# Performance work log

Measured on AMD Instinct MI355X. Metric: run time of the kernel, lower is better.

## Reference

```python
import jax, jax.numpy as jnp
import numpy as np

N = 100000       # nodes
F_IN = 512       # input features
H = 16           # hidden dim of conv1
C = 5            # num classes
E = 6400000      # edges (avg degree 64)


def setup_inputs() -> dict:
    key = jax.random.key(0)
    ks = jax.random.split(key, 8)
    x = jax.random.normal(ks[0], (N, F_IN), dtype=jnp.float32)
    edge_index = jax.random.randint(ks[1], (2, E), 0, N, dtype=jnp.int64)
    W1 = jax.random.normal(ks[2], (F_IN, H), dtype=jnp.float32) * (1.0 / np.sqrt(F_IN))
    b1 = jnp.zeros((H,), jnp.float32)
    W2 = jax.random.normal(ks[3], (H, C), dtype=jnp.float32) * (1.0 / np.sqrt(H))
    b2 = jnp.zeros((C,), jnp.float32)
    W3 = jax.random.normal(ks[4], (C, 32), dtype=jnp.float32) * (1.0 / np.sqrt(C))
    b3 = jnp.zeros((32,), jnp.float32)
    W4 = jax.random.normal(ks[5], (32, C), dtype=jnp.float32) * (1.0 / np.sqrt(32))
    b4 = jnp.zeros((C,), jnp.float32)
    return {"x": x, "edge_index": edge_index, "W1": W1, "b1": b1,
            "W2": W2, "b2": b2, "W3": W3, "b3": b3, "W4": W4, "b4": b4}


def _gcn_norm(edge_index):
    # add self-loops, unit edge weights (data has no edge_attr)
    loop = jnp.arange(N, dtype=edge_index.dtype)
    src = jnp.concatenate([edge_index[0], loop])
    dst = jnp.concatenate([edge_index[1], loop])
    deg = jax.ops.segment_sum(jnp.ones_like(dst, dtype=jnp.float32), dst,
                              num_segments=N)
    dinv = jnp.where(deg > 0, jax.lax.rsqrt(jnp.maximum(deg, 1.0)), 0.0)
    norm = dinv[src] * dinv[dst]  # [E+N]
    return src, dst, norm


def _gcn_conv(x, src, dst, norm, W, b):
    h = x @ W                               # transform first (small out dim)
    msg = h[src] * norm[:, None]            # gather + edge-normalize
    out = jax.ops.segment_sum(msg, dst, num_segments=N)  # scatter-add
    return out + b


def reference(x, edge_index, W1, b1, W2, b2, W3, b3, W4, b4):
    src, dst, norm = _gcn_norm(edge_index)
    h = _gcn_conv(x, src, dst, norm, W1, b1)
    h = jax.nn.relu(h)
    # F.dropout(training=self.training): identity in eval mode
    h = _gcn_conv(h, src, dst, norm, W2, b2)
    h = jax.nn.relu(h @ W3 + b3)
    h = h @ W4 + b4
    return jax.nn.log_softmax(h, axis=1)
```

## Files before the change

kernel.cpp:

```cpp
#include <hip/hip_runtime.h>
#include <hip/hip_bf16.h>


#define F_IN 512
#define HDIM 16
#define CDIM 5
#define NB   1024
#define SEG  8192
#define GWP_STRIDE 16
#define SCHUNK 12288
#define CAP  8192

typedef __attribute__((ext_vector_type(8))) short short8;
typedef __attribute__((ext_vector_type(4))) float floatx4;

__device__ inline float bf2f(unsigned short u){
  unsigned int i = ((unsigned int)u) << 16; float f; __builtin_memcpy(&f, &i, 4); return f;
}
__device__ inline unsigned short f2bf(float x){
  unsigned int i; __builtin_memcpy(&i, &x, 4);
  unsigned int r = i + 0x7FFFu + ((i >> 16) & 1u);
  return (unsigned short)(r >> 16);
}
__device__ inline float ulo(unsigned int u){
  unsigned int v = u << 16; float f; __builtin_memcpy(&f, &v, 4); return f;
}
__device__ inline float uhi(unsigned int u){
  unsigned int v = u & 0xFFFF0000u; float f; __builtin_memcpy(&f, &v, 4); return f;
}
__device__ inline short8 pack8(float4 u0, float4 u1){
  unsigned short o[8] = {f2bf(u0.x), f2bf(u0.y), f2bf(u0.z), f2bf(u0.w),
                         f2bf(u1.x), f2bf(u1.y), f2bf(u1.z), f2bf(u1.w)};
  short8 r; __builtin_memcpy(&r, o, 16); return r;
}

__global__ void k_detect(const int* __restrict__ ei, int* __restrict__ flag,
                         int* __restrict__ gwp, int E){
  int k = blockIdx.x * blockDim.x + threadIdx.x;
  if (k < NB) gwp[k * GWP_STRIDE] = k * SEG;
  long long step = E / 2048; if (step < 1) step = 1;
  long long pos = 2LL * ((long long)k * step) + 1;
  if (pos < 2LL * E){
    if (ei[pos] != 0) atomicOr(flag, 1);
  }
}

__global__ __launch_bounds__(1024) void k_binscatter(const int* __restrict__ ei, const int* __restrict__ flag,
                                                     int* __restrict__ gwp, int* __restrict__ pairs,
                                                     int E, int NPB){
  __shared__ int bh[NB];
  __shared__ int lex[NB + 1];
  __shared__ int bb2[NB];
  __shared__ int wsum[16];
  __shared__ int stage[SCHUNK];
  int t = threadIdx.x;
  int e0 = blockIdx.x * SCHUNK;
  int e1 = min(E, e0 + SCHUNK);
  int cnt = e1 - e0;
  if (cnt <= 0) return;
  int is32 = *flag;
  const uint2* ei2 = (const uint2*)ei;
  bh[t] = 0;
  __syncthreads();
  for (int e = e0 + t; e < e1; e += 1024){
    int dst = is32 ? ei[(size_t)E + e] : (int)ei2[(size_t)E + e].x;
    atomicAdd(&bh[dst / NPB], 1);
  }
  __syncthreads();
  {
    int lane = t & 63, w = t >> 6;
    int v = bh[t];
    int xs = v;
    #pragma unroll
    for (int off = 1; off < 64; off <<= 1){
      int y = __shfl_up(xs, off);
      if (lane >= off) xs += y;
    }
    if (lane == 63) wsum[w] = xs;
    __syncthreads();
    int woff = 0;
    for (int k = 0; k < w; ++k) woff += wsum[k];
    int excl = woff + xs - v;
    lex[t] = excl;
    if (t == 1023) lex[NB] = woff + xs;
    bb2[t] = v ? atomicAdd(&gwp[t * GWP_STRIDE], v) : 0;
    __syncthreads();
    bh[t] = excl;
  }
  __syncthreads();
  for (int e = e0 + t; e < e1; e += 1024){
    int src, dst;
    if (is32){ src = ei[e]; dst = ei[(size_t)E + e]; }
    else     { src = (int)ei2[e].x; dst = (int)ei2[(size_t)E + e].x; }
    int b = dst / NPB;
    int dl = dst - b * NPB;
    int idx = atomicAdd(&bh[b], 1);
    stage[idx] = src | (dl << 20);
  }
  __syncthreads();
  for (int k = t; k < cnt; k += 1024){
    int lo = 0, hi = NB;
    while (hi - lo > 1){
      int mid = (lo + hi) >> 1;
      if (lex[mid] <= k) lo = mid; else hi = mid;
    }
    pairs[bb2[lo] + (k - lex[lo])] = stage[k];
  }
}

__global__ __launch_bounds__(1024) void k_scanNB(const int* __restrict__ gwp, int* __restrict__ bbase,
                                                 int nb){
  __shared__ int wsum[16];
  int t = threadIdx.x, lane = t & 63, w = t >> 6;
  int v = (t < nb) ? (gwp[t * GWP_STRIDE] - t * SEG) : 0;
  int xs = v;
  #pragma unroll
  for (int off = 1; off < 64; off <<= 1){
    int y = __shfl_up(xs, off);
    if (lane >= off) xs += y;
  }
  if (lane == 63) wsum[w] = xs;
  __syncthreads();
  int woff = 0;
  for (int k = 0; k < w; ++k) woff += wsum[k];
  if (t < nb) bbase[t] = woff + xs - v;
  if (t == 1023) bbase[nb] = woff + xs;
}

__global__ __launch_bounds__(512) void k_bucket(const int* __restrict__ pairs, const int* __restrict__ bbase,
                                                int* __restrict__ rowptr, float* __restrict__ dinv,
                                                int* __restrict__ ssrc, int NPB, int n, int Etot){
  __shared__ int lcnt[4][128];
  __shared__ int tot[128];
  __shared__ int lexcl[129];
  __shared__ int stage[CAP];
  int b = blockIdx.x;
  int t = threadIdx.x;
  int g = t >> 7;
  int node0 = b * NPB;
  int pbase = b * SEG;
  int obase = bbase[b];
  int cntE = bbase[b + 1] - obase;
  lcnt[g][t & 127] = 0;
  __syncthreads();
  for (int k = t; k < cntE; k += 512){
    unsigned int v = (unsigned int)pairs[pbase + k];
    atomicAdd(&lcnt[g][v >> 20], 1);
  }
  __syncthreads();
  if (t < 128){
    int s0 = lcnt[0][t], s1 = lcnt[1][t], s2 = lcnt[2][t], s3 = lcnt[3][t];
    tot[t] = s0 + s1 + s2 + s3;
    lcnt[0][t] = 0; lcnt[1][t] = s0; lcnt[2][t] = s0 + s1; lcnt[3][t] = s0 + s1 + s2;
  }
  __syncthreads();
  if (t == 0){
    int s = 0;
    for (int k = 0; k < NPB; ++k){ lexcl[k] = s; s += tot[k]; }
    lexcl[NPB] = s;
  }
  __syncthreads();
  if (t < NPB){
    int node = node0 + t;
    if (node < n){
      rowptr[node] = obase + lexcl[t];
      dinv[node] = rsqrtf((float)(tot[t] + 1));
    }
  }
  lcnt[g][t & 127] += lexcl[t & 127];
  if (b == 0 && t == 0) rowptr[n] = Etot;
  __syncthreads();
  for (int k = t; k < cntE; k += 512){
    unsigned int v = (unsigned int)pairs[pbase + k];
    int idx = atomicAdd(&lcnt[g][v >> 20], 1);
    int src = (int)(v & 0xFFFFFu);
    if (idx < CAP) stage[idx] = src;
    else ssrc[obase + idx] = src;
  }
  __syncthreads();
  int m = cntE < CAP ? cntE : CAP;
  for (int k = t; k < m; k += 512) ssrc[obase + k] = stage[k];
}

__global__ __launch_bounds__(256) void k_gemm1(const float* __restrict__ x, const float* __restrict__ W1,
                                               const float* __restrict__ dinv, unsigned short* __restrict__ hs1,
                                               int n){
  int lane = threadIdx.x & 63;
  int col = lane & 15;
  int kg  = lane >> 4;
  int nt = (n + 15) >> 4;
  short8 B[16];
  #pragma unroll
  for (int t = 0; t < 16; ++t){
    unsigned short o[8];
    #pragma unroll
    for (int e = 0; e < 8; ++e)
      o[e] = f2bf(W1[(t * 32 + kg * 8 + e) * HDIM + col]);
    __builtin_memcpy(&B[t], o, 16);
  }
  int nw = gridDim.x * 4;
  for (int wid = blockIdx.x * 4 + (threadIdx.x >> 6); wid < nt; wid += nw){
    int row = wid * 16 + col;
    const float* xr = x + (size_t)min(row, n - 1) * F_IN;
    floatx4 acc = {0.f, 0.f, 0.f, 0.f};
    #pragma unroll
    for (int t = 0; t < 16; ++t){
      const float4* p = (const float4*)(xr + t * 32 + kg * 8);
      float4 u0 = p[0];
      float4 u1 = p[1];
      acc = __builtin_amdgcn_mfma_f32_16x16x32_bf16(pack8(u0, u1), B[t], acc, 0, 0, 0);
    }
    #pragma unroll
    for (int r = 0; r < 4; ++r){
      int orow = wid * 16 + kg * 4 + r;
      if (orow < n) hs1[(size_t)orow * HDIM + col] = f2bf(dinv[orow] * acc[r]);
    }
  }
}

__global__ __launch_bounds__(256) void k_agg1(const unsigned short* __restrict__ hs1,
    const int* __restrict__ rowptr, const int* __restrict__ ssrc,
    const float* __restrict__ dinv, const float* __restrict__ b1,
    const float* __restrict__ W2, unsigned short* __restrict__ hs2, int n){
  int lane = threadIdx.x & 63;
  int i = blockIdx.x * 4 + (threadIdx.x >> 6);
  if (i >= n) return;
  int slot = lane >> 1, half = lane & 1;
  int beg = rowptr[i], end = rowptr[i + 1];
  const uint4* hv = (const uint4*)hs1;
  float acc[8];
  #pragma unroll
  for (int k = 0; k < 8; ++k) acc[k] = 0.f;
  for (int e = beg + slot; e < end; e += 32){
    int src = ssrc[e];
    uint4 v = hv[(size_t)src * 2 + half];
    acc[0] += ulo(v.x); acc[1] += uhi(v.x);
    acc[2] += ulo(v.y); acc[3] += uhi(v.y);
    acc[4] += ulo(v.z); acc[5] += uhi(v.z);
    acc[6] += ulo(v.w); acc[7] += uhi(v.w);
  }
  #pragma unroll
  for (int off = 2; off < 64; off <<= 1){
    #pragma unroll
    for (int k = 0; k < 8; ++k) acc[k] += __shfl_xor(acc[k], off);
  }
  uint4 sv = hv[(size_t)i * 2 + half];
  float self[8] = {ulo(sv.x), uhi(sv.x), ulo(sv.y), uhi(sv.y),
                   ulo(sv.z), uhi(sv.z), ulo(sv.w), uhi(sv.w)};
  float dv = dinv[i];
  const float4* b1v = (const float4*)b1;
  float4 bl = b1v[half * 2], bh = b1v[half * 2 + 1];
  float r[8];
  r[0] = fmaxf(fmaf(dv, acc[0] + self[0], bl.x), 0.f);
  r[1] = fmaxf(fmaf(dv, acc[1] + self[1], bl.y), 0.f);
  r[2] = fmaxf(fmaf(dv, acc[2] + self[2], bl.z), 0.f);
  r[3] = fmaxf(fmaf(dv, acc[3] + self[3], bl.w), 0.f);
  r[4] = fmaxf(fmaf(dv, acc[4] + self[4], bh.x), 0.f);
  r[5] = fmaxf(fmaf(dv, acc[5] + self[5], bh.y), 0.f);
  r[6] = fmaxf(fmaf(dv, acc[6] + self[6], bh.z), 0.f);
  r[7] = fmaxf(fmaf(dv, acc[7] + self[7], bh.w), 0.f);
  const float* w2 = W2 + half * 8 * CDIM;
  float p[CDIM];
  #pragma unroll
  for (int c = 0; c < CDIM; ++c){
    float s = 0.f;
    #pragma unroll
    for (int k = 0; k < 8; ++k) s = fmaf(r[k], w2[k * CDIM + c], s);
    p[c] = s;
  }
  #pragma unroll
  for (int c = 0; c < CDIM; ++c) p[c] += __shfl_xor(p[c], 1);
  if (lane == 0){
    unsigned short o[8];
    #pragma unroll
    for (int c = 0; c < CDIM; ++c) o[c] = f2bf(dv * p[c]);
    o[5] = 0; o[6] = 0; o[7] = 0;
    uint4 v; __builtin_memcpy(&v, o, 16);
    *(uint4*)(hs2 + (size_t)i * 8) = v;
  }
}

__global__ __launch_bounds__(256) void k_agg2(const unsigned short* __restrict__ hs2,
    const int* __restrict__ rowptr, const int* __restrict__ ssrc,
    const float* __restrict__ dinv, const float* __restrict__ b2,
    const float* __restrict__ W3, const float* __restrict__ b3,
    const float* __restrict__ W4, const float* __restrict__ b4,
    float* __restrict__ out, int n){
  int lane = threadIdx.x & 63;
  int i = blockIdx.x * 4 + (threadIdx.x >> 6);
  if (i >= n) return;
  int beg = rowptr[i], end = rowptr[i + 1];
  const uint4* hv = (const uint4*)hs2;
  float acc[CDIM];
  #pragma unroll
  for (int k = 0; k < CDIM; ++k) acc[k] = 0.f;
  for (int e = beg + lane; e < end; e += 64){
    int src = ssrc[e];
    uint4 v = hv[src];
    acc[0] += ulo(v.x); acc[1] += uhi(v.x);
    acc[2] += ulo(v.y); acc[3] += uhi(v.y);
    acc[4] += ulo(v.z);
  }
  #pragma unroll
  for (int off = 1; off < 64; off <<= 1){
    #pragma unroll
    for (int k = 0; k < CDIM; ++k) acc[k] += __shfl_xor(acc[k], off);
  }
  float dv = dinv[i];
  uint4 sv = hv[i];
  float a0 = fmaf(dv, acc[0] + ulo(sv.x), b2[0]);
  float a1 = fmaf(dv, acc[1] + uhi(sv.x), b2[1]);
  float a2 = fmaf(dv, acc[2] + ulo(sv.y), b2[2]);
  float a3 = fmaf(dv, acc[3] + uhi(sv.y), b2[3]);
  float a4 = fmaf(dv, acc[4] + ulo(sv.z), b2[4]);
  int m = lane & 31;
  float h3 = b3[m];
  h3 = fmaf(a0, W3[0 * 32 + m], h3);
  h3 = fmaf(a1, W3[1 * 32 + m], h3);
  h3 = fmaf(a2, W3[2 * 32 + m], h3);
  h3 = fmaf(a3, W3[3 * 32 + m], h3);
  h3 = fmaf(a4, W3[4 * 32 + m], h3);
  h3 = fmaxf(h3, 0.f);
  float q0 = h3 * W4[m * CDIM + 0], q1 = h3 * W4[m * CDIM + 1], q2 = h3 * W4[m * CDIM + 2];
  float q3 = h3 * W4[m * CDIM + 3], q4 = h3 * W4[m * CDIM + 4];
  #pragma unroll
  for (int off = 1; off < 32; off <<= 1){
    q0 += __shfl_xor(q0, off); q1 += __shfl_xor(q1, off); q2 += __shfl_xor(q2, off);
    q3 += __shfl_xor(q3, off); q4 += __shfl_xor(q4, off);
  }
  q0 += b4[0]; q1 += b4[1]; q2 += b4[2]; q3 += b4[3]; q4 += b4[4];
  float mx = fmaxf(fmaxf(fmaxf(q0, q1), fmaxf(q2, q3)), q4);
  float sum = expf(q0 - mx) + expf(q1 - mx) + expf(q2 - mx) + expf(q3 - mx) + expf(q4 - mx);
  float lse = mx + logf(sum);
  if (lane < CDIM){
    float v = q0;
    if (lane == 1) v = q1;
    if (lane == 2) v = q2;
    if (lane == 3) v = q3;
    if (lane == 4) v = q4;
    out[(size_t)i * CDIM + lane] = v - lse;
  }
}

extern "C" void kernel_launch(void* const* d_in, const int* in_sizes, int n_in,
                              void* d_out, int out_size, void* d_ws, size_t ws_size,
                              hipStream_t stream){
  const float* x  = (const float*)d_in[0];
  const int*   ei = (const int*)d_in[1];
  const float* W1 = (const float*)d_in[2];
  const float* b1 = (const float*)d_in[3];
  const float* W2 = (const float*)d_in[4];
  const float* b2 = (const float*)d_in[5];
  const float* W3 = (const float*)d_in[6];
  const float* b3 = (const float*)d_in[7];
  const float* W4 = (const float*)d_in[8];
  const float* b4 = (const float*)d_in[9];
  float* out = (float*)d_out;

  int N = in_sizes[0] / F_IN;
  int E = in_sizes[1] / 2;
  int NPB = (N + NB - 1) / NB;

  char* ws = (char*)d_ws;
  size_t off = 0;
  auto alloc = [&](size_t bytes) -> char* {
    char* p = ws + off;
    off += (bytes + 255) & ~(size_t)255;
    return p;
  };
  int* flag  = (int*)alloc(4);
  int* gwp   = (int*)alloc((size_t)NB * GWP_STRIDE * 4);
  int* bbase = (int*)alloc(((size_t)NB + 1) * 4);
  int* rowptr= (int*)alloc(((size_t)N + 1) * 4);
  float* dinv= (float*)alloc((size_t)N * 4);
  int* pairs = (int*)alloc((size_t)NB * SEG * 4);
  int* ssrc  = (int*)alloc((size_t)E * 4);
  unsigned short* hs1 = (unsigned short*)alloc((size_t)N * HDIM * 2);
  unsigned short* hs2 = (unsigned short*)alloc((size_t)N * 8 * 2);
  (void)ws_size; (void)n_in; (void)out_size;

  hipMemsetAsync(flag, 0, 4, stream);
  k_detect<<<8, 256, 0, stream>>>(ei, flag, gwp, E);
  int sblocks = (E + SCHUNK - 1) / SCHUNK;
  k_binscatter<<<sblocks, 1024, 0, stream>>>(ei, flag, gwp, pairs, E, NPB);
  k_scanNB<<<1, 1024, 0, stream>>>(gwp, bbase, NB);
  k_bucket<<<NB, 512, 0, stream>>>(pairs, bbase, rowptr, dinv, ssrc, NPB, N, E);
  k_gemm1<<<768, 256, 0, stream>>>(x, W1, dinv, hs1, N);
  k_agg1<<<(N + 3) / 4, 256, 0, stream>>>(hs1, rowptr, ssrc, dinv, b1, W2, hs2, N);
  k_agg2<<<(N + 3) / 4, 256, 0, stream>>>(hs2, rowptr, ssrc, dinv, b2, W3, b3, W4, b4, out, N);
}
```

Baseline: 282.3 us.

## Load edges once into registers in binscatter, parallel scan in bucket, drop memset

The binscatter kernel now reads each edge's src/dst once into per-thread register arrays (12 per thread) and reuses them for both the histogram and scatter passes, instead of reading edge_index twice from global memory. The bucket kernel replaces a serial single-thread prefix sum over node counts with a wave-shuffle scan. The flag memset is folded into a single-block detect kernel, removing one launch. The register arrays raise register pressure in a 1024-thread block, and the in-kernel flag clear relies on __syncthreads ordering within that one block.

```diff
diff --git a/kernel.cpp b/kernel.cpp
--- a/kernel.cpp
+++ b/kernel.cpp
@@ -8,7 +8,8 @@
 #define NB   1024
 #define SEG  8192
 #define GWP_STRIDE 16
-#define SCHUNK 12288
+#define EPT  12
+#define SCHUNK (1024*EPT)
 #define CAP  8192
 
 typedef __attribute__((ext_vector_type(8))) short short8;
@@ -34,12 +35,14 @@
   short8 r; __builtin_memcpy(&r, o, 16); return r;
 }
 
-__global__ void k_detect(const int* __restrict__ ei, int* __restrict__ flag,
-                         int* __restrict__ gwp, int E){
-  int k = blockIdx.x * blockDim.x + threadIdx.x;
-  if (k < NB) gwp[k * GWP_STRIDE] = k * SEG;
-  long long step = E / 2048; if (step < 1) step = 1;
-  long long pos = 2LL * ((long long)k * step) + 1;
+__global__ __launch_bounds__(1024) void k_detect(const int* __restrict__ ei, int* __restrict__ flag,
+                                                 int* __restrict__ gwp, int E){
+  int t = threadIdx.x;
+  if (t == 0) *flag = 0;
+  gwp[t * GWP_STRIDE] = t * SEG;
+  __syncthreads();
+  long long step = E / 1024; if (step < 1) step = 1;
+  long long pos = 2LL * ((long long)t * step) + 1;
   if (pos < 2LL * E){
     if (ei[pos] != 0) atomicOr(flag, 1);
   }
@@ -60,12 +63,23 @@
   if (cnt <= 0) return;
   int is32 = *flag;
   const uint2* ei2 = (const uint2*)ei;
+  int pk[EPT]; int bi[EPT];
+  #pragma unroll
+  for (int j = 0; j < EPT; ++j){
+    int e = e0 + t + j * 1024;
+    if (e < e1){
+      int src, dst;
+      if (is32){ src = ei[e]; dst = ei[(size_t)E + e]; }
+      else     { src = (int)ei2[e].x; dst = (int)ei2[(size_t)E + e].x; }
+      int b = dst / NPB;
+      pk[j] = src | ((dst - b * NPB) << 20);
+      bi[j] = b;
+    } else bi[j] = -1;
+  }
   bh[t] = 0;
   __syncthreads();
-  for (int e = e0 + t; e < e1; e += 1024){
-    int dst = is32 ? ei[(size_t)E + e] : (int)ei2[(size_t)E + e].x;
-    atomicAdd(&bh[dst / NPB], 1);
-  }
+  #pragma unroll
+  for (int j = 0; j < EPT; ++j) if (bi[j] >= 0) atomicAdd(&bh[bi[j]], 1);
   __syncthreads();
   {
     int lane = t & 63, w = t >> 6;
@@ -88,14 +102,12 @@
     bh[t] = excl;
   }
   __syncthreads();
-  for (int e = e0 + t; e < e1; e += 1024){
-    int src, dst;
-    if (is32){ src = ei[e]; dst = ei[(size_t)E + e]; }
-    else     { src = (int)ei2[e].x; dst = (int)ei2[(size_t)E + e].x; }
-    int b = dst / NPB;
-    int dl = dst - b * NPB;
-    int idx = atomicAdd(&bh[b], 1);
-    stage[idx] = src | (dl << 20);
+  #pragma unroll
+  for (int j = 0; j < EPT; ++j){
+    if (bi[j] >= 0){
+      int idx = atomicAdd(&bh[bi[j]], 1);
+      stage[idx] = pk[j];
+    }
   }
   __syncthreads();
   for (int k = t; k < cnt; k += 1024){
@@ -132,7 +144,8 @@
                                                 int* __restrict__ ssrc, int NPB, int n, int Etot){
   __shared__ int lcnt[4][128];
   __shared__ int tot[128];
-  __shared__ int lexcl[129];
+  __shared__ int lexcl[128];
+  __shared__ int w0sum;
   __shared__ int stage[CAP];
   int b = blockIdx.x;
   int t = threadIdx.x;
@@ -154,11 +167,17 @@
     lcnt[0][t] = 0; lcnt[1][t] = s0; lcnt[2][t] = s0 + s1; lcnt[3][t] = s0 + s1 + s2;
   }
   __syncthreads();
-  if (t == 0){
-    int s = 0;
-    for (int k = 0; k < NPB; ++k){ lexcl[k] = s; s += tot[k]; }
-    lexcl[NPB] = s;
-  }
+  int lane = t & 63;
+  int v = (t < 128) ? tot[t] : 0;
+  int xs = v;
+  #pragma unroll
+  for (int off = 1; off < 64; off <<= 1){
+    int y = __shfl_up(xs, off);
+    if (lane >= off) xs += y;
+  }
+  if (t == 63) w0sum = xs;
+  __syncthreads();
+  if (t < 128) lexcl[t] = xs - v + ((t >= 64) ? w0sum : 0);
   __syncthreads();
   if (t < NPB){
     int node = node0 + t;
@@ -171,9 +190,9 @@
   if (b == 0 && t == 0) rowptr[n] = Etot;
   __syncthreads();
   for (int k = t; k < cntE; k += 512){
-    unsigned int v = (unsigned int)pairs[pbase + k];
-    int idx = atomicAdd(&lcnt[g][v >> 20], 1);
-    int src = (int)(v & 0xFFFFFu);
+    unsigned int v2 = (unsigned int)pairs[pbase + k];
+    int idx = atomicAdd(&lcnt[g][v2 >> 20], 1);
+    int src = (int)(v2 & 0xFFFFFu);
     if (idx < CAP) stage[idx] = src;
     else ssrc[obase + idx] = src;
   }
@@ -379,8 +398,7 @@
   unsigned short* hs2 = (unsigned short*)alloc((size_t)N * 8 * 2);
   (void)ws_size; (void)n_in; (void)out_size;
 
-  hipMemsetAsync(flag, 0, 4, stream);
-  k_detect<<<8, 256, 0, stream>>>(ei, flag, gwp, E);
+  k_detect<<<1, 1024, 0, stream>>>(ei, flag, gwp, E);
   int sblocks = (E + SCHUNK - 1) / SCHUNK;
   k_binscatter<<<sblocks, 1024, 0, stream>>>(ei, flag, gwp, pairs, E, NPB);
   k_scanNB<<<1, 1024, 0, stream>>>(gwp, bbase, NB);
```

New measurement: 273.8 us. 3.0% less time.
